# Kernel optimization log

Measured on AMD Instinct MI355X. Metric: run time of the kernel, lower is better.

Reference implementation:

```python
import jax, jax.numpy as jnp
import numpy as np

N_HEADS = 16
LOCAL_WINDOW = 512
ROPE_BASE = 10000.0


def _rotate_half(x):
    # interleaved rotate: out[..., 2i] = -x[..., 2i+1], out[..., 2i+1] = x[..., 2i]
    x1 = x[..., 0::2]
    x2 = x[..., 1::2]
    return jnp.stack((-x2, x1), axis=-1).reshape(x.shape)


def _rope_cache(T, hd, dtype):
    half = hd // 2
    inv_freq = 1.0 / (ROPE_BASE ** (jnp.arange(half, dtype=dtype) / half))
    t = jnp.arange(T, dtype=dtype)
    freqs = t[:, None] * inv_freq[None, :]  # [T, half]
    cos = jnp.repeat(jnp.cos(freqs), 2, axis=-1)  # [T, hd]
    sin = jnp.repeat(jnp.sin(freqs), 2, axis=-1)
    return cos, sin


def setup_inputs() -> dict:
    key = jax.random.key(0)
    k1, k2, k3, k4 = jax.random.split(key, 4)
    B, T, C = 2, 2048, 1024
    x = jax.random.normal(k1, (B, T, C), dtype=jnp.float32)
    Wqkv = jax.random.normal(k2, (3 * C, C), dtype=jnp.float32) * 0.02
    Wproj = jax.random.normal(k3, (C, C), dtype=jnp.float32) * 0.02
    bproj = jax.random.normal(k4, (C,), dtype=jnp.float32) * 0.02
    return {"x": x, "Wqkv": Wqkv, "Wproj": Wproj, "bproj": bproj}


def reference(x, Wqkv, Wproj, bproj):
    B, T, C = x.shape
    H = N_HEADS
    hd = C // H
    qkv = (x @ Wqkv.T).reshape(B, T, 3, H, hd).transpose(2, 0, 3, 1, 4)  # [3,B,H,T,hd]
    q, k, v = qkv[0], qkv[1], qkv[2]
    cos, sin = _rope_cache(T, hd, x.dtype)
    cos = cos[None, None]  # [1,1,T,hd]
    sin = sin[None, None]
    q = q * cos + _rotate_half(q) * sin
    k = k * cos + _rotate_half(k) * sin
    scale = 1.0 / jnp.sqrt(jnp.asarray(hd, dtype=x.dtype))
    scores = jnp.einsum('bhqd,bhkd->bhqk', q, k) * scale  # [B,H,T,T]
    i = jnp.arange(T)[:, None]
    j = jnp.arange(T)[None, :]
    allow = (j <= i) & (jnp.abs(i - j) <= LOCAL_WINDOW)  # causal & local band
    scores = jnp.where(allow[None, None], scores, jnp.asarray(-jnp.inf, dtype=x.dtype))
    attn = jax.nn.softmax(scores, axis=-1)
    y = jnp.einsum('bhqk,bhkd->bhqd', attn, v)  # [B,H,T,hd]
    y = y.transpose(0, 2, 1, 3).reshape(B, T, C)
    return y @ Wproj.T + bproj
```

## Files before the change

kernel.cpp:

```cpp
#include <hip/hip_runtime.h>
#include <math.h>

#define B_   2
#define T_   2048
#define C_   1024
#define H_   16
#define HD_  64
#define WIN_ 512
#define BT_  (B_ * T_)

typedef __bf16 bf16x8 __attribute__((ext_vector_type(8)));
typedef float  f32x4  __attribute__((ext_vector_type(4)));
typedef unsigned int u32x2 __attribute__((ext_vector_type(2)));
typedef unsigned short u16x8 __attribute__((ext_vector_type(8)));

__device__ __forceinline__ f32x4 mfma16(bf16x8 a, bf16x8 b, f32x4 c) {
    return __builtin_amdgcn_mfma_f32_16x16x32_bf16(a, b, c, 0, 0, 0);
}
__device__ __forceinline__ unsigned short f2b(float f) {
    __bf16 h = (__bf16)f;
    unsigned short u;
    __builtin_memcpy(&u, &h, 2);
    return u;
}
__device__ __forceinline__ void async_copy16(__bf16* lds, const __bf16* g) {
    __builtin_amdgcn_global_load_lds(
        (const __attribute__((address_space(1))) void*)g,
        (__attribute__((address_space(3))) void*)lds,
        16, 0, 0);
}

#define TR16(dst, va, OFFLIT) \
    asm volatile("ds_read_b64_tr_b16 %0, %1 offset:" OFFLIT : "=v"(dst) : "v"(va))

__device__ __forceinline__ bf16x8 combine_tr(u32x2 a, u32x2 b) {
    union { unsigned u[4]; bf16x8 v; } x;
    x.u[0] = a[0]; x.u[1] = a[1]; x.u[2] = b[0]; x.u[3] = b[1];
    return x.v;
}

#define VMW(n) asm volatile("s_waitcnt vmcnt(" #n ")" ::: "memory")

__global__ void prep_k(const float* __restrict__ x, const float* __restrict__ Wqkv,
                       const float* __restrict__ Wproj,
                       __bf16* __restrict__ xb, __bf16* __restrict__ Wqkvb,
                       __bf16* __restrict__ Wprojb,
                       float* __restrict__ cosT, float* __restrict__ sinT) {
    const int gid = blockIdx.x * 256 + threadIdx.x;
    const int N0 = BT_ * 1024 / 8;
    const int N1 = N0 + 3072 * 1024 / 8;
    const int N2 = N1 + 1024 * 1024 / 8;
    const int N3 = N2 + T_ * 32 / 8;
    if (gid < N2) {
        const float* src; __bf16* dst; int off;
        if (gid < N0)      { src = x;     dst = xb;     off = gid; }
        else if (gid < N1) { src = Wqkv;  dst = Wqkvb;  off = gid - N0; }
        else               { src = Wproj; dst = Wprojb; off = gid - N1; }
        float4 a = *(const float4*)&src[(size_t)off * 8];
        float4 b = *(const float4*)&src[(size_t)off * 8 + 4];
        bf16x8 o;
        o[0] = (__bf16)a.x; o[1] = (__bf16)a.y; o[2] = (__bf16)a.z; o[3] = (__bf16)a.w;
        o[4] = (__bf16)b.x; o[5] = (__bf16)b.y; o[6] = (__bf16)b.z; o[7] = (__bf16)b.w;
        *(bf16x8*)&dst[(size_t)off * 8] = o;
    } else if (gid < N3) {
        const int r = gid - N2;
        #pragma unroll
        for (int e = 0; e < 8; ++e) {
            int idx = r * 8 + e;
            int t = idx >> 5, j = idx & 31;
            float inv = powf(10000.0f, -(float)j / 32.0f);
            float f = (float)t * inv;
            cosT[idx] = cosf(f);
            sinT[idx] = sinf(f);
        }
    }
}

__global__ __launch_bounds__(256) void gemm_qkv_rope(
        const __bf16* __restrict__ A, const __bf16* __restrict__ Bm,
        __bf16* __restrict__ Cv, int M, int N, int K,
        const float* __restrict__ cosT, const float* __restrict__ sinT)
{
    __shared__ __bf16 sA[3][128 * 32];
    __shared__ __bf16 sB[3][128 * 32];
    const int tid  = threadIdx.x;
    const int w    = tid >> 6;
    const int lane = tid & 63;
    const int c    = lane & 15;
    const int g    = lane >> 4;
    const int bm0  = blockIdx.y * 128;
    const int bn0  = blockIdx.x * 128;
    const int wm0  = (w >> 1) * 64;
    const int wn0  = (w & 1) * 64;

    f32x4 acc[4][4] = {};

    auto stage = [&](int buf, int k0) {
        #pragma unroll
        for (int it = 0; it < 2; ++it) {
            int s   = it * 256 + tid;
            int row = s >> 2;
            int col = ((s & 3) ^ ((row >> 1) & 3)) * 8;
            async_copy16(&sA[buf][s * 8], &A[(size_t)(bm0 + row) * K + k0 + col]);
            async_copy16(&sB[buf][s * 8], &Bm[(size_t)(bn0 + row) * K + k0 + col]);
        }
    };

    const int NT = K >> 5;
    stage(0, 0);
    stage(1, 32);

    int cons = 0;
    for (int t = 0; t < NT; ++t) {
        if (t + 1 < NT) { VMW(4); } else { VMW(0); }
        __builtin_amdgcn_sched_barrier(0);
        __builtin_amdgcn_s_barrier();
        if (t + 2 < NT) {
            int fill = cons + 2; if (fill >= 3) fill -= 3;
            stage(fill, (t + 2) * 32);
        }
        const __bf16* cA = sA[cons];
        const __bf16* cB = sB[cons];
        bf16x8 af[4], bfr[4];
        #pragma unroll
        for (int m = 0; m < 4; ++m) {
            int r = wm0 + m * 16 + c;
            af[m] = *(const bf16x8*)&cA[r * 32 + ((g ^ ((r >> 1) & 3)) * 8)];
        }
        #pragma unroll
        for (int n = 0; n < 4; ++n) {
            int r = wn0 + n * 16 + c;
            bfr[n] = *(const bf16x8*)&cB[r * 32 + ((g ^ ((r >> 1) & 3)) * 8)];
        }
        __builtin_amdgcn_s_setprio(1);
        #pragma unroll
        for (int m = 0; m < 4; ++m)
            #pragma unroll
            for (int n = 0; n < 4; ++n)
                acc[m][n] = mfma16(af[m], bfr[n], acc[m][n]);
        __builtin_amdgcn_s_setprio(0);
        cons = (cons + 1 == 3) ? 0 : cons + 1;
    }

    #pragma unroll
    for (int m = 0; m < 4; ++m) {
        #pragma unroll
        for (int r2 = 0; r2 < 4; ++r2) {
            const int row = bm0 + wm0 + m * 16 + g * 4 + r2;
            const int t = row & (T_ - 1);
            #pragma unroll
            for (int n = 0; n < 4; ++n) {
                const int cbase = bn0 + wn0 + n * 16;
                const int cc = cbase + c;
                float v = acc[m][n][r2];
                float outv;
                if (cbase < 2048) {
                    float prt = __shfl_xor(v, 1);
                    int jj = (cc & 63) >> 1;
                    float cs = cosT[t * 32 + jj];
                    float sn = sinT[t * 32 + jj];
                    outv = (cc & 1) ? (v * cs + prt * sn) : (v * cs - prt * sn);
                } else {
                    outv = v;
                }
                Cv[(size_t)row * N + cc] = (__bf16)outv;
            }
        }
    }
}

__global__ __launch_bounds__(256) void gemm64_proj(
        const __bf16* __restrict__ A, const __bf16* __restrict__ Bm,
        const float* __restrict__ bias, float* __restrict__ Cv,
        int M, int N, int K)
{
    __shared__ __bf16 sA[3][64 * 32];
    __shared__ __bf16 sB[3][64 * 32];
    const int tid  = threadIdx.x;
    const int w    = tid >> 6;
    const int lane = tid & 63;
    const int c    = lane & 15;
    const int g    = lane >> 4;

    const int nbx = N >> 6;
    const int cpx = gridDim.x >> 3;
    const int bid = blockIdx.x;
    const int swz = (bid & 7) * cpx + (bid >> 3);
    const int bm0 = (swz / nbx) << 6;
    const int bn0 = (swz % nbx) << 6;
    const int wm  = (w >> 1) << 5;
    const int wn  = (w & 1) << 5;

    f32x4 acc[2][2] = {};

    const int srow = tid >> 2;
    const int schk = tid & 3;
    const int scol = (schk ^ ((srow >> 1) & 3)) * 8;
    const int sdst = (srow * 4 + schk) * 8;

    auto stage = [&](int buf, int k0) {
        async_copy16(&sA[buf][sdst], &A[(size_t)(bm0 + srow) * K + k0 + scol]);
        async_copy16(&sB[buf][sdst], &Bm[(size_t)(bn0 + srow) * K + k0 + scol]);
    };

    const int NT = K >> 5;
    stage(0, 0);
    stage(1, 32);

    int cons = 0;
    for (int t = 0; t < NT; ++t) {
        if (t + 1 < NT) { VMW(2); } else { VMW(0); }
        __builtin_amdgcn_sched_barrier(0);
        __builtin_amdgcn_s_barrier();
        if (t + 2 < NT) {
            int fill = cons + 2; if (fill >= 3) fill -= 3;
            stage(fill, (t + 2) * 32);
        }
        const __bf16* cA = sA[cons];
        const __bf16* cB = sB[cons];
        bf16x8 af[2], bfr[2];
        #pragma unroll
        for (int m = 0; m < 2; ++m) {
            int r = wm + m * 16 + c;
            af[m] = *(const bf16x8*)&cA[r * 32 + ((g ^ ((r >> 1) & 3)) * 8)];
        }
        #pragma unroll
        for (int n = 0; n < 2; ++n) {
            int r = wn + n * 16 + c;
            bfr[n] = *(const bf16x8*)&cB[r * 32 + ((g ^ ((r >> 1) & 3)) * 8)];
        }
        __builtin_amdgcn_s_setprio(1);
        #pragma unroll
        for (int m = 0; m < 2; ++m)
            #pragma unroll
            for (int n = 0; n < 2; ++n)
                acc[m][n] = mfma16(af[m], bfr[n], acc[m][n]);
        __builtin_amdgcn_s_setprio(0);
        cons = (cons + 1 == 3) ? 0 : cons + 1;
    }

    #pragma unroll
    for (int m = 0; m < 2; ++m) {
        int rr = bm0 + wm + m * 16 + g * 4;
        #pragma unroll
        for (int n = 0; n < 2; ++n) {
            int cc = bn0 + wn + n * 16 + c;
            float bv = bias[cc];
            #pragma unroll
            for (int r2 = 0; r2 < 4; ++r2)
                Cv[(size_t)(rr + r2) * N + cc] = acc[m][n][r2] + bv;
        }
    }
}

__global__ __launch_bounds__(256) void attn_k(const __bf16* __restrict__ qkv,
                                              __bf16* __restrict__ y)
{
    __shared__ __align__(16) unsigned short Ks[2][64 * 72];
    __shared__ __align__(16) unsigned short Vs[2][4 * 1040];
    __shared__ __align__(16) unsigned short Ps[64 * 72];

    const int tid  = threadIdx.x;
    const int lane = tid & 63;
    const int w    = tid >> 6;
    const int c    = lane & 15;
    const int g    = lane >> 4;

    const int bid = blockIdx.x;
    const int swz = (bid & 7) * 128 + (bid >> 3);
    const int q0 = (swz & 31) * 64;
    const int hb = swz >> 5;
    const int h  = hb & 15;
    const int b  = hb >> 4;

    bf16x8 qa[2];
    {
        const int qrow = q0 + w * 16 + c;
        const __bf16* qp = qkv + (size_t)(b * T_ + qrow) * 3072 + h * 64 + g * 8;
        bf16x8 r0 = *(const bf16x8*)qp;
        bf16x8 r1 = *(const bf16x8*)(qp + 32);
        #pragma unroll
        for (int e = 0; e < 8; ++e) {
            qa[0][e] = (__bf16)((float)r0[e] * 0.125f);
            qa[1][e] = (__bf16)((float)r1[e] * 0.125f);
        }
    }

    float m_run[4] = {-1e30f, -1e30f, -1e30f, -1e30f};
    float l_run[4] = {0.f, 0.f, 0.f, 0.f};
    f32x4 o[4] = {};

    unsigned vs_lane;
    {
        auto* p3 = (__attribute__((address_space(3))) const unsigned short*)&Vs[0][0];
        vs_lane = (unsigned)(unsigned long long)p3 + (unsigned)(g * 256 + c * 8);
    }

    const int r0s = tid >> 3,          d80 = (tid & 7) * 8;
    const int r1s = (tid + 256) >> 3,  d81 = d80;
    const size_t kbase = (size_t)(b * T_) * 3072 + 1024 + h * 64;

    const int j_start = (q0 >= WIN_) ? (q0 - WIN_) : 0;

    u16x8 kr0, kr1, vr0, vr1;
    {
        const __bf16* p0 = qkv + kbase + (size_t)(j_start + r0s) * 3072 + d80;
        const __bf16* p1 = qkv + kbase + (size_t)(j_start + r1s) * 3072 + d81;
        kr0 = *(const u16x8*)p0;  vr0 = *(const u16x8*)(p0 + 1024);
        kr1 = *(const u16x8*)p1;  vr1 = *(const u16x8*)(p1 + 1024);
    }

    int cur = 0;
    for (int j0 = j_start; j0 <= q0; j0 += 64) {
        {
            union { u16x8 v; ushort4 h[2]; } u;
            u.v = kr0;
            *(ushort4*)&Ks[cur][r0s * 72 + d80]     = u.h[0];
            *(ushort4*)&Ks[cur][r0s * 72 + d80 + 4] = u.h[1];
            u.v = kr1;
            *(ushort4*)&Ks[cur][r1s * 72 + d81]     = u.h[0];
            *(ushort4*)&Ks[cur][r1s * 72 + d81 + 4] = u.h[1];
            *(u16x8*)&Vs[cur][(d80 >> 4) * 1040 + r0s * 16 + (d80 & 15)] = vr0;
            *(u16x8*)&Vs[cur][(d81 >> 4) * 1040 + r1s * 16 + (d81 & 15)] = vr1;
        }
        __syncthreads();

        if (j0 + 64 <= q0) {
            const __bf16* p0 = qkv + kbase + (size_t)(j0 + 64 + r0s) * 3072 + d80;
            const __bf16* p1 = qkv + kbase + (size_t)(j0 + 64 + r1s) * 3072 + d81;
            kr0 = *(const u16x8*)p0;  vr0 = *(const u16x8*)(p0 + 1024);
            kr1 = *(const u16x8*)p1;  vr1 = *(const u16x8*)(p1 + 1024);
        }

        f32x4 sc[4];
        __builtin_amdgcn_s_setprio(1);
        #pragma unroll
        for (int nt = 0; nt < 4; ++nt) {
            const bf16x8 b0 = *(const bf16x8*)&Ks[cur][(nt * 16 + c) * 72 + g * 8];
            const bf16x8 b1 = *(const bf16x8*)&Ks[cur][(nt * 16 + c) * 72 + 32 + g * 8];
            f32x4 s = {0.f, 0.f, 0.f, 0.f};
            s = mfma16(qa[0], b0, s);
            s = mfma16(qa[1], b1, s);
            sc[nt] = s;
        }
        __builtin_amdgcn_s_setprio(0);

        const int rlo = q0 + w * 16;
        const bool need_mask = (j0 + 63 > rlo) || (rlo + 15 - j0 > WIN_);
        if (need_mask) {
            #pragma unroll
            for (int reg = 0; reg < 4; ++reg) {
                const int i_abs = rlo + g * 4 + reg;
                #pragma unroll
                for (int nt = 0; nt < 4; ++nt) {
                    int j_abs = j0 + nt * 16 + c;
                    bool ok = (j_abs <= i_abs) && (i_abs - j_abs <= WIN_);
                    sc[nt][reg] = ok ? sc[nt][reg] : -1e30f;
                }
            }
        }

        float pmax[4];
        #pragma unroll
        for (int reg = 0; reg < 4; ++reg) {
            float bm = fmaxf(fmaxf(sc[0][reg], sc[1][reg]), fmaxf(sc[2][reg], sc[3][reg]));
            #pragma unroll
            for (int off = 1; off < 16; off <<= 1)
                bm = fmaxf(bm, __shfl_xor(bm, off));
            pmax[reg] = bm;
        }
        int need = 0;
        #pragma unroll
        for (int reg = 0; reg < 4; ++reg)
            need |= (pmax[reg] > m_run[reg] + 8.f) ? 1 : 0;
        if (__any(need)) {
            #pragma unroll
            for (int reg = 0; reg < 4; ++reg) {
                float mn = fmaxf(m_run[reg], pmax[reg]);
                float corr = __expf(m_run[reg] - mn);
                m_run[reg] = mn;
                l_run[reg] *= corr;
                #pragma unroll
                for (int dt = 0; dt < 4; ++dt) o[dt][reg] *= corr;
            }
        }
        #pragma unroll
        for (int reg = 0; reg < 4; ++reg) {
            #pragma unroll
            for (int nt = 0; nt < 4; ++nt) {
                float p = __expf(sc[nt][reg] - m_run[reg]);
                l_run[reg] += p;
                Ps[(w * 16 + g * 4 + reg) * 72 + nt * 16 + c] = f2b(p);
            }
        }

        const bf16x8 pa0 = *(const bf16x8*)&Ps[(w * 16 + c) * 72 + g * 8];
        const bf16x8 pa1 = *(const bf16x8*)&Ps[(w * 16 + c) * 72 + 32 + g * 8];
        u32x2 t0[4], t1[4], t2[4], t3[4];
        #pragma unroll
        for (int dt = 0; dt < 4; ++dt) {
            unsigned va = vs_lane + (unsigned)cur * 8320u + dt * 2080;
            TR16(t0[dt], va, "0");
            TR16(t1[dt], va, "128");
            TR16(t2[dt], va, "1024");
            TR16(t3[dt], va, "1152");
        }
        asm volatile("s_waitcnt lgkmcnt(0)" ::: "memory");
        __builtin_amdgcn_sched_barrier(0);
        __builtin_amdgcn_s_setprio(1);
        #pragma unroll
        for (int dt = 0; dt < 4; ++dt) {
            bf16x8 vb0 = combine_tr(t0[dt], t1[dt]);
            bf16x8 vb1 = combine_tr(t2[dt], t3[dt]);
            o[dt] = mfma16(pa0, vb0, o[dt]);
            o[dt] = mfma16(pa1, vb1, o[dt]);
        }
        __builtin_amdgcn_s_setprio(0);
        cur ^= 1;
    }

    float inv_l[4];
    #pragma unroll
    for (int reg = 0; reg < 4; ++reg) {
        float L = l_run[reg];
        #pragma unroll
        for (int off = 1; off < 16; off <<= 1)
            L += __shfl_xor(L, off);
        inv_l[reg] = 1.f / L;
    }
    #pragma unroll
    for (int dt = 0; dt < 4; ++dt)
        #pragma unroll
        for (int reg = 0; reg < 4; ++reg) {
            size_t row = (size_t)(b * T_ + q0 + w * 16 + g * 4 + reg);
            y[row * 1024 + h * 64 + dt * 16 + c] = (__bf16)(o[dt][reg] * inv_l[reg]);
        }
}

extern "C" void kernel_launch(void* const* d_in, const int* in_sizes, int n_in,
                              void* d_out, int out_size, void* d_ws, size_t ws_size,
                              hipStream_t stream) {
    const float* x     = (const float*)d_in[0];
    const float* Wqkv  = (const float*)d_in[1];
    const float* Wproj = (const float*)d_in[2];
    const float* bproj = (const float*)d_in[3];
    float* out = (float*)d_out;

    char* p = (char*)d_ws;
    float*  cosT   = (float*)p;   p += (size_t)T_ * 32 * 4;
    float*  sinT   = (float*)p;   p += (size_t)T_ * 32 * 4;
    __bf16* xb     = (__bf16*)p;  p += (size_t)BT_ * 1024 * 2;
    __bf16* Wqkvb  = (__bf16*)p;  p += (size_t)3072 * 1024 * 2;
    __bf16* Wprojb = (__bf16*)p;  p += (size_t)1024 * 1024 * 2;
    __bf16* qkvb   = (__bf16*)p;  p += (size_t)BT_ * 3072 * 2;
    __bf16* yb     = (__bf16*)p;  p += (size_t)BT_ * 1024 * 2;

    const int nprep = (BT_ * 1024 + 3072 * 1024 + 1024 * 1024) / 8 + T_ * 32 / 8;
    prep_k<<<(nprep + 255) / 256, 256, 0, stream>>>(
        x, Wqkv, Wproj, xb, Wqkvb, Wprojb, cosT, sinT);

    dim3 g1(3072 / 128, BT_ / 128);
    gemm_qkv_rope<<<g1, 256, 0, stream>>>(
        xb, Wqkvb, qkvb, BT_, 3072, 1024, cosT, sinT);

    attn_k<<<(T_ / 64) * H_ * B_, 256, 0, stream>>>(qkvb, yb);

    gemm64_proj<<<(BT_ / 64) * (1024 / 64), 256, 0, stream>>>(
        yb, Wprojb, bproj, out, BT_, 1024, 1024);
}
```

Measured before the change: 118.3 us.

## Shrink attention KV tile to 32 and swizzle QKV GEMM block order

The attention kernel now walks keys in 32-row tiles instead of 64 and stops at q0+32. Near the diagonal this skips more fully masked columns, and the K/V shared buffers shrink, which may allow higher occupancy. The cost is twice as many loop iterations, each with its own barrier, online-softmax update and shuffle reductions. Separately, the QKV GEMM moves to a 1D grid with a block-ID swizzle so that concurrently running blocks share A and B tiles in L2.

After: 114.5 us, median of 3. -3.3%, faster.

```diff
diff --git a/kernel.cpp b/kernel.cpp
--- a/kernel.cpp
+++ b/kernel.cpp
@@ -88,10 +88,15 @@
     const int lane = tid & 63;
     const int c    = lane & 15;
     const int g    = lane >> 4;
-    const int bm0  = blockIdx.y * 128;
-    const int bn0  = blockIdx.x * 128;
-    const int wm0  = (w >> 1) * 64;
-    const int wn0  = (w & 1) * 64;
+
+    const int nbx = N >> 7;
+    const int cpx = gridDim.x >> 3;
+    const int bid = blockIdx.x;
+    const int swz = (bid & 7) * cpx + (bid >> 3);
+    const int bm0 = (swz / nbx) << 7;
+    const int bn0 = (swz % nbx) << 7;
+    const int wm0 = (w >> 1) * 64;
+    const int wn0 = (w & 1) * 64;
 
     f32x4 acc[4][4] = {};
 
@@ -256,8 +261,8 @@
 __global__ __launch_bounds__(256) void attn_k(const __bf16* __restrict__ qkv,
                                               __bf16* __restrict__ y)
 {
-    __shared__ __align__(16) unsigned short Ks[2][64 * 72];
-    __shared__ __align__(16) unsigned short Vs[2][4 * 1040];
+    __shared__ __align__(16) unsigned short Ks[2][32 * 72];
+    __shared__ __align__(16) unsigned short Vs[2][4 * 528];
     __shared__ __align__(16) unsigned short Ps[64 * 72];
 
     const int tid  = threadIdx.x;
@@ -296,46 +301,33 @@
         vs_lane = (unsigned)(unsigned long long)p3 + (unsigned)(g * 256 + c * 8);
     }
 
-    const int r0s = tid >> 3,          d80 = (tid & 7) * 8;
-    const int r1s = (tid + 256) >> 3,  d81 = d80;
+    const int rs = tid >> 3, d8 = (tid & 7) * 8;
     const size_t kbase = (size_t)(b * T_) * 3072 + 1024 + h * 64;
 
     const int j_start = (q0 >= WIN_) ? (q0 - WIN_) : 0;
-
-    u16x8 kr0, kr1, vr0, vr1;
+    const int j_end   = q0 + 32;
+
+    u16x8 kr, vr;
     {
-        const __bf16* p0 = qkv + kbase + (size_t)(j_start + r0s) * 3072 + d80;
-        const __bf16* p1 = qkv + kbase + (size_t)(j_start + r1s) * 3072 + d81;
-        kr0 = *(const u16x8*)p0;  vr0 = *(const u16x8*)(p0 + 1024);
-        kr1 = *(const u16x8*)p1;  vr1 = *(const u16x8*)(p1 + 1024);
+        const __bf16* p0 = qkv + kbase + (size_t)(j_start + rs) * 3072 + d8;
+        kr = *(const u16x8*)p0;  vr = *(const u16x8*)(p0 + 1024);
     }
 
     int cur = 0;
-    for (int j0 = j_start; j0 <= q0; j0 += 64) {
-        {
-            union { u16x8 v; ushort4 h[2]; } u;
-            u.v = kr0;
-            *(ushort4*)&Ks[cur][r0s * 72 + d80]     = u.h[0];
-            *(ushort4*)&Ks[cur][r0s * 72 + d80 + 4] = u.h[1];
-            u.v = kr1;
-            *(ushort4*)&Ks[cur][r1s * 72 + d81]     = u.h[0];
-            *(ushort4*)&Ks[cur][r1s * 72 + d81 + 4] = u.h[1];
-            *(u16x8*)&Vs[cur][(d80 >> 4) * 1040 + r0s * 16 + (d80 & 15)] = vr0;
-            *(u16x8*)&Vs[cur][(d81 >> 4) * 1040 + r1s * 16 + (d81 & 15)] = vr1;
-        }
+    for (int j0 = j_start; j0 <= j_end; j0 += 32) {
+        *(u16x8*)&Ks[cur][rs * 72 + d8] = kr;
+        *(u16x8*)&Vs[cur][(d8 >> 4) * 528 + rs * 16 + (d8 & 15)] = vr;
         __syncthreads();
 
-        if (j0 + 64 <= q0) {
-            const __bf16* p0 = qkv + kbase + (size_t)(j0 + 64 + r0s) * 3072 + d80;
-            const __bf16* p1 = qkv + kbase + (size_t)(j0 + 64 + r1s) * 3072 + d81;
-            kr0 = *(const u16x8*)p0;  vr0 = *(const u16x8*)(p0 + 1024);
-            kr1 = *(const u16x8*)p1;  vr1 = *(const u16x8*)(p1 + 1024);
-        }
-
-        f32x4 sc[4];
+        if (j0 + 32 <= j_end) {
+            const __bf16* p0 = qkv + kbase + (size_t)(j0 + 32 + rs) * 3072 + d8;
+            kr = *(const u16x8*)p0;  vr = *(const u16x8*)(p0 + 1024);
+        }
+
+        f32x4 sc[2];
         __builtin_amdgcn_s_setprio(1);
         #pragma unroll
-        for (int nt = 0; nt < 4; ++nt) {
+        for (int nt = 0; nt < 2; ++nt) {
             const bf16x8 b0 = *(const bf16x8*)&Ks[cur][(nt * 16 + c) * 72 + g * 8];
             const bf16x8 b1 = *(const bf16x8*)&Ks[cur][(nt * 16 + c) * 72 + 32 + g * 8];
             f32x4 s = {0.f, 0.f, 0.f, 0.f};
@@ -346,13 +338,13 @@
         __builtin_amdgcn_s_setprio(0);
 
         const int rlo = q0 + w * 16;
-        const bool need_mask = (j0 + 63 > rlo) || (rlo + 15 - j0 > WIN_);
+        const bool need_mask = (j0 + 31 > rlo) || (rlo + 15 - j0 > WIN_);
         if (need_mask) {
             #pragma unroll
             for (int reg = 0; reg < 4; ++reg) {
                 const int i_abs = rlo + g * 4 + reg;
                 #pragma unroll
-                for (int nt = 0; nt < 4; ++nt) {
+                for (int nt = 0; nt < 2; ++nt) {
                     int j_abs = j0 + nt * 16 + c;
                     bool ok = (j_abs <= i_abs) && (i_abs - j_abs <= WIN_);
                     sc[nt][reg] = ok ? sc[nt][reg] : -1e30f;
@@ -363,7 +355,7 @@
         float pmax[4];
         #pragma unroll
         for (int reg = 0; reg < 4; ++reg) {
-            float bm = fmaxf(fmaxf(sc[0][reg], sc[1][reg]), fmaxf(sc[2][reg], sc[3][reg]));
+            float bm = fmaxf(sc[0][reg], sc[1][reg]);
             #pragma unroll
             for (int off = 1; off < 16; off <<= 1)
                 bm = fmaxf(bm, __shfl_xor(bm, off));
@@ -387,33 +379,28 @@
         #pragma unroll
         for (int reg = 0; reg < 4; ++reg) {
             #pragma unroll
-            for (int nt = 0; nt < 4; ++nt) {
+            for (int nt = 0; nt < 2; ++nt) {
                 float p = __expf(sc[nt][reg] - m_run[reg]);
                 l_run[reg] += p;
                 Ps[(w * 16 + g * 4 + reg) * 72 + nt * 16 + c] = f2b(p);
             }
         }
 
-        const bf16x8 pa0 = *(const bf16x8*)&Ps[(w * 16 + c) * 72 + g * 8];
-        const bf16x8 pa1 = *(const bf16x8*)&Ps[(w * 16 + c) * 72 + 32 + g * 8];
-        u32x2 t0[4], t1[4], t2[4], t3[4];
+        const bf16x8 pa = *(const bf16x8*)&Ps[(w * 16 + c) * 72 + g * 8];
+        u32x2 t0[4], t1[4];
         #pragma unroll
         for (int dt = 0; dt < 4; ++dt) {
-            unsigned va = vs_lane + (unsigned)cur * 8320u + dt * 2080;
+            unsigned va = vs_lane + (unsigned)cur * 4224u + dt * 1056u;
             TR16(t0[dt], va, "0");
             TR16(t1[dt], va, "128");
-            TR16(t2[dt], va, "1024");
-            TR16(t3[dt], va, "1152");
         }
         asm volatile("s_waitcnt lgkmcnt(0)" ::: "memory");
         __builtin_amdgcn_sched_barrier(0);
         __builtin_amdgcn_s_setprio(1);
         #pragma unroll
         for (int dt = 0; dt < 4; ++dt) {
-            bf16x8 vb0 = combine_tr(t0[dt], t1[dt]);
-            bf16x8 vb1 = combine_tr(t2[dt], t3[dt]);
-            o[dt] = mfma16(pa0, vb0, o[dt]);
-            o[dt] = mfma16(pa1, vb1, o[dt]);
+            bf16x8 vb = combine_tr(t0[dt], t1[dt]);
+            o[dt] = mfma16(pa, vb, o[dt]);
         }
         __builtin_amdgcn_s_setprio(0);
         cur ^= 1;
@@ -459,8 +446,7 @@
     prep_k<<<(nprep + 255) / 256, 256, 0, stream>>>(
         x, Wqkv, Wproj, xb, Wqkvb, Wprojb, cosT, sinT);
 
-    dim3 g1(3072 / 128, BT_ / 128);
-    gemm_qkv_rope<<<g1, 256, 0, stream>>>(
+    gemm_qkv_rope<<<(BT_ / 128) * (3072 / 128), 256, 0, stream>>>(
         xb, Wqkvb, qkvb, BT_, 3072, 1024, cosT, sinT);
 
     attn_k<<<(T_ / 64) * H_ * B_, 256, 0, stream>>>(qkvb, yb);
```
